# Kernel optimization log

Measured on AMD Instinct MI355X. Metric: run time of the kernel, lower is better.

The kernel has to match this reference:

```python
import jax, jax.numpy as jnp
import numpy as np

INPUT_DIM = 512
PROJ_DIM = 128
HIDDEN = INPUT_DIM // 2  # 256


def setup_inputs() -> dict:
    key = jax.random.key(0)
    ks = jax.random.split(key, 6)
    B = 8192
    s1 = 1.0 / np.sqrt(INPUT_DIM)
    s2 = 1.0 / np.sqrt(HIDDEN)
    return {
        "fused_text": jax.random.normal(ks[0], (B, INPUT_DIM), dtype=jnp.float32),
        "x": jax.random.normal(ks[1], (B, INPUT_DIM), dtype=jnp.float32),
        # generator layer 1: Linear(input_dim, input_dim//2), torch layout [out, in]
        "W1": jax.random.uniform(ks[2], (HIDDEN, INPUT_DIM), jnp.float32, -s1, s1),
        "b1": jax.random.uniform(ks[3], (HIDDEN,), jnp.float32, -s1, s1),
        # generator layer 2: Linear(input_dim//2, proj_dim * input_dim)
        "W2": jax.random.uniform(ks[4], (PROJ_DIM * INPUT_DIM, HIDDEN), jnp.float32, -s2, s2),
        "b2": jax.random.uniform(ks[5], (PROJ_DIM * INPUT_DIM,), jnp.float32, -s2, s2),
    }


def reference(fused_text, x, W1, b1, W2, b2):
    B = fused_text.shape[0]
    # hypernetwork generator MLP
    h = jax.nn.relu(fused_text @ W1.T + b1)          # [B, hidden]
    w_flat = h @ W2.T + b2                           # [B, proj_dim * input_dim]
    W = w_flat.reshape(B, PROJ_DIM, INPUT_DIM)       # per-sample weights
    # per-sample projection: bmm(W, x[..., None]).squeeze(-1)
    out = jnp.einsum("bpi,bi->bp", W, x)             # [B, proj_dim]
    return out
```

## Files before the change

kernel.cpp:

```cpp
#include <hip/hip_runtime.h>
#include <stdint.h>

#define B_SZ   8192
#define IN_DIM 512
#define HID    256
#define PROJ   128

typedef __attribute__((ext_vector_type(8))) short bf16x8;
typedef __attribute__((ext_vector_type(4))) float f32x4;

#define GLDS16(gp, lp) __builtin_amdgcn_global_load_lds( \
    (const __attribute__((address_space(1))) void*)(gp), \
    (__attribute__((address_space(3))) void*)(lp), 16, 0, 0)

__device__ __forceinline__ unsigned short f2bf(float f) {
    union { float f; uint32_t u; } c; c.f = f;
    uint32_t u = c.u;
    uint32_t r = (u + 0x7fffu + ((u >> 16) & 1u)) >> 16;
    return (unsigned short)r;
}
__device__ __forceinline__ float bfhi(uint32_t v) {
    union { uint32_t u; float f; } c; c.u = v & 0xffff0000u; return c.f;
}
__device__ __forceinline__ float bflo(uint32_t v) {
    union { uint32_t u; float f; } c; c.u = v << 16; return c.f;
}

__global__ __launch_bounds__(256) void k0_prep(
        const float4* __restrict__ W2, ushort4* __restrict__ W2b,
        const float* __restrict__ x, unsigned short* __restrict__ xTb) {
    __shared__ float tile[64][65];
    const int bid = blockIdx.x;
    if (bid < 2048) {
        const int nW2 = (PROJ * IN_DIM * HID) / 4;
        const int stride = 2048 * 256;
        for (int i = bid * 256 + threadIdx.x; i < nW2; i += stride) {
            float4 v = W2[i];
            ushort4 o;
            o.x = f2bf(v.x); o.y = f2bf(v.y); o.z = f2bf(v.z); o.w = f2bf(v.w);
            W2b[i] = o;
        }
    } else {
        const int tb = bid - 2048;
        const int bi = tb & 7, bb = tb >> 3;
        const int i0 = bi * 64, b0 = bb * 64;
        const int t = threadIdx.x;
        const int c = t & 63, r4 = t >> 6;
        #pragma unroll
        for (int rr = 0; rr < 64; rr += 4)
            tile[rr + r4][c] = x[(size_t)(b0 + rr + r4) * IN_DIM + i0 + c];
        __syncthreads();
        #pragma unroll
        for (int rr = 0; rr < 64; rr += 4)
            xTb[(size_t)(i0 + rr + r4) * B_SZ + b0 + c] = f2bf(tile[c][rr + r4]);
    }
}

__device__ __forceinline__ bf16x8 ld_cvt8(const float* __restrict__ s) {
    float4 a = *(const float4*)s;
    float4 b = *(const float4*)(s + 4);
    bf16x8 r;
    r[0] = (short)f2bf(a.x); r[1] = (short)f2bf(a.y);
    r[2] = (short)f2bf(a.z); r[3] = (short)f2bf(a.w);
    r[4] = (short)f2bf(b.x); r[5] = (short)f2bf(b.y);
    r[6] = (short)f2bf(b.z); r[7] = (short)f2bf(b.w);
    return r;
}

__global__ __launch_bounds__(256) void k1_hidden(
        const float* __restrict__ ft,
        const float* __restrict__ W1,
        const float* __restrict__ b1,
        unsigned short* __restrict__ hb) {
    const int lane = threadIdx.x & 63;
    const int wv   = threadIdx.x >> 6;
    const int l15  = lane & 15, q = lane >> 4;
    const int b0 = blockIdx.x * 32;
    const int n0 = wv * 64;

    f32x4 acc[2][4];
    const f32x4 z4 = {0.f, 0.f, 0.f, 0.f};
    #pragma unroll
    for (int mt = 0; mt < 2; ++mt)
        #pragma unroll
        for (int nt = 0; nt < 4; ++nt) acc[mt][nt] = z4;

    for (int kq = 0; kq < 16; ++kq) {
        const int koff = kq * 32 + q * 8;
        bf16x8 a[2], bb[4];
        #pragma unroll
        for (int mt = 0; mt < 2; ++mt)
            a[mt] = ld_cvt8(ft + (size_t)(b0 + mt*16 + l15) * IN_DIM + koff);
        #pragma unroll
        for (int nt = 0; nt < 4; ++nt)
            bb[nt] = ld_cvt8(W1 + (size_t)(n0 + nt*16 + l15) * IN_DIM + koff);
        #pragma unroll
        for (int mt = 0; mt < 2; ++mt)
            #pragma unroll
            for (int nt = 0; nt < 4; ++nt)
                acc[mt][nt] = __builtin_amdgcn_mfma_f32_16x16x32_bf16(
                    a[mt], bb[nt], acc[mt][nt], 0, 0, 0);
    }
    #pragma unroll
    for (int nt = 0; nt < 4; ++nt) {
        float bias = b1[n0 + nt*16 + l15];
        #pragma unroll
        for (int mt = 0; mt < 2; ++mt)
            #pragma unroll
            for (int r = 0; r < 4; ++r) {
                float v = acc[mt][nt][r] + bias;
                v = fmaxf(v, 0.f);
                hb[(size_t)(b0 + mt*16 + q*4 + r) * HID + n0 + nt*16 + l15] = f2bf(v);
            }
    }
}

__global__ __launch_bounds__(256) void k2_bias(
        const float* __restrict__ x,
        const float* __restrict__ b2,
        float* __restrict__ out) {
    const int lane = threadIdx.x & 63;
    const int wv   = threadIdx.x >> 6;
    const int l15  = lane & 15, q = lane >> 4;
    const int b0 = blockIdx.x * 32;
    const int n0 = wv * 32;

    f32x4 acc[2][2];
    const f32x4 z4 = {0.f, 0.f, 0.f, 0.f};
    #pragma unroll
    for (int mt = 0; mt < 2; ++mt)
        #pragma unroll
        for (int nt = 0; nt < 2; ++nt) acc[mt][nt] = z4;

    for (int kq = 0; kq < 16; ++kq) {
        const int koff = kq * 32 + q * 8;
        bf16x8 a[2], bb[2];
        #pragma unroll
        for (int mt = 0; mt < 2; ++mt)
            a[mt] = ld_cvt8(x + (size_t)(b0 + mt*16 + l15) * IN_DIM + koff);
        #pragma unroll
        for (int nt = 0; nt < 2; ++nt)
            bb[nt] = ld_cvt8(b2 + (size_t)(n0 + nt*16 + l15) * IN_DIM + koff);
        #pragma unroll
        for (int mt = 0; mt < 2; ++mt)
            #pragma unroll
            for (int nt = 0; nt < 2; ++nt)
                acc[mt][nt] = __builtin_amdgcn_mfma_f32_16x16x32_bf16(
                    a[mt], bb[nt], acc[mt][nt], 0, 0, 0);
    }
    #pragma unroll
    for (int mt = 0; mt < 2; ++mt)
        #pragma unroll
        for (int nt = 0; nt < 2; ++nt)
            #pragma unroll
            for (int r = 0; r < 4; ++r)
                out[(size_t)(b0 + mt*16 + q*4 + r) * PROJ + n0 + nt*16 + l15]
                    = acc[mt][nt][r];
}

__global__ __launch_bounds__(256, 3) void k3_main(
        const unsigned short* __restrict__ W2b,
        const unsigned short* __restrict__ hb,
        const unsigned short* __restrict__ xTb,
        float* __restrict__ out) {
    __shared__ unsigned short w2t[2][64 * 128];
    __shared__ unsigned short xt[2][32 * 128];
    const int tid  = threadIdx.x;
    const int lane = tid & 63;
    const int wv   = tid >> 6;
    const int l15  = lane & 15, q = lane >> 4;
    const int pgrp = blockIdx.x & 63;
    const int bsup = blockIdx.x >> 6;
    const int p0   = pgrp * 2;
    const int b0blk = bsup * 128;
    const int b0w  = b0blk + wv * 32;
    const f32x4 z4 = {0.f, 0.f, 0.f, 0.f};

    bf16x8 afr[2][8];
    #pragma unroll
    for (int mt = 0; mt < 2; ++mt) {
        const unsigned short* hrow = hb + (size_t)(b0w + mt*16 + l15) * HID + q * 8;
        #pragma unroll
        for (int kk = 0; kk < 8; ++kk)
            afr[mt][kk] = *(const bf16x8*)(hrow + kk * 32);
    }

    const int grow = lane >> 4;
    const int cbase = (lane & 15) ^ grow;
    const unsigned short* wsp[4];
    #pragma unroll
    for (int jj = 0; jj < 4; ++jj) {
        const int j   = wv*4 + jj;
        const int row = j*4 + grow;
        const int c   = cbase ^ (4*(jj & 1));
        wsp[jj] = W2b + ((size_t)(p0 + (row >> 5)) * IN_DIM + (row & 31)) * HID + c * 8;
    }
    const unsigned short* xsp[2];
    #pragma unroll
    for (int jj = 0; jj < 2; ++jj) {
        const int j2  = wv*2 + jj;
        const int row = j2*4 + (lane >> 4);
        const int g   = (lane & 15) ^ (row & 7);
        xsp[jj] = xTb + (size_t)row * B_SZ + b0blk + g * 8;
    }

    float oacc[2][2][4];
    #pragma unroll
    for (int pp = 0; pp < 2; ++pp)
        #pragma unroll
        for (int mt = 0; mt < 2; ++mt)
            #pragma unroll
            for (int r = 0; r < 4; ++r) oacc[pp][mt][r] = 0.f;

#define STAGE(BUFI, TT) do {                                              \
    const int _kh = (TT) >> 4, _ic = (TT) & 15;                           \
    const size_t _wadd = (size_t)(_ic * 32) * HID + _kh * 128;            \
    const size_t _xadd = (size_t)(_ic * 32) * B_SZ;                       \
    unsigned short* _Lw = &w2t[BUFI][0];                                  \
    unsigned short* _Lx = &xt[BUFI][0];                                   \
    _Pragma("unroll")                                                     \
    for (int _jj = 0; _jj < 4; ++_jj)                                     \
        GLDS16(wsp[_jj] + _wadd, _Lw + (wv*4 + _jj) * 512);               \
    _Pragma("unroll")                                                     \
    for (int _jj = 0; _jj < 2; ++_jj)                                     \
        GLDS16(xsp[_jj] + _xadd, _Lx + (wv*2 + _jj) * 512);               \
} while (0)

#define COMPUTE(KHC) do {                                                 \
    _Pragma("unroll")                                                     \
    for (int sub = 0; sub < 2; ++sub) {                                   \
        const int rloc = sub*16 + l15;                                    \
        uint2 xv[2];                                                      \
        _Pragma("unroll")                                                 \
        for (int mt = 0; mt < 2; ++mt) {                                  \
            const int gch = wv*4 + mt*2 + (q >> 1);                       \
            const int pos = gch ^ (rloc & 7);                             \
            xv[mt] = *(const uint2*)(Lx + rloc*128 + pos*8 + (q & 1)*4);  \
        }                                                                 \
        _Pragma("unroll")                                                 \
        for (int pp = 0; pp < 2; ++pp) {                                  \
            const unsigned short* Bp = Lw + (pp*32 + rloc) * 128;         \
            const int sw = rloc & 7;                                      \
            bf16x8 bfr[4];                                                \
            _Pragma("unroll")                                             \
            for (int kq = 0; kq < 4; ++kq)                                \
                bfr[kq] = *(const bf16x8*)(Bp + (((q + 4*kq) ^ sw)) * 8); \
            f32x4 D[2];                                                   \
            _Pragma("unroll")                                             \
            for (int mt = 0; mt < 2; ++mt)                                \
                D[mt] = __builtin_amdgcn_mfma_f32_16x16x32_bf16(          \
                    afr[mt][(KHC)*4 + 0], bfr[0], z4, 0, 0, 0);           \
            _Pragma("unroll")                                             \
            for (int kq = 1; kq < 4; ++kq)                                \
                _Pragma("unroll")                                         \
                for (int mt = 0; mt < 2; ++mt)                            \
                    D[mt] = __builtin_amdgcn_mfma_f32_16x16x32_bf16(      \
                        afr[mt][(KHC)*4 + kq], bfr[kq], D[mt], 0, 0, 0);  \
            _Pragma("unroll")                                             \
            for (int mt = 0; mt < 2; ++mt) {                              \
                oacc[pp][mt][0] = fmaf(D[mt][0], bflo(xv[mt].x), oacc[pp][mt][0]); \
                oacc[pp][mt][1] = fmaf(D[mt][1], bfhi(xv[mt].x), oacc[pp][mt][1]); \
                oacc[pp][mt][2] = fmaf(D[mt][2], bflo(xv[mt].y), oacc[pp][mt][2]); \
                oacc[pp][mt][3] = fmaf(D[mt][3], bfhi(xv[mt].y), oacc[pp][mt][3]); \
            }                                                             \
        }                                                                 \
    }                                                                     \
} while (0)

    STAGE(0, 0);
    STAGE(1, 1);

    #pragma unroll 1
    for (int t = 0; t < 32; ++t) {
        if (t < 31) asm volatile("s_waitcnt vmcnt(6)" ::: "memory");
        else        asm volatile("s_waitcnt vmcnt(0)" ::: "memory");
        __builtin_amdgcn_s_barrier();
        asm volatile("" ::: "memory");

        const unsigned short* Lw = &w2t[t & 1][0];
        const unsigned short* Lx = &xt[t & 1][0];
        if (t < 16) COMPUTE(0);
        else        COMPUTE(1);

        asm volatile("" ::: "memory");
        __builtin_amdgcn_s_barrier();
        asm volatile("" ::: "memory");

        if (t < 30) {
            const int tn = t + 2;
            STAGE(tn & 1, tn);
        }
    }
#undef STAGE
#undef COMPUTE

    #pragma unroll
    for (int pp = 0; pp < 2; ++pp)
        #pragma unroll
        for (int mt = 0; mt < 2; ++mt)
            #pragma unroll
            for (int r = 0; r < 4; ++r) {
                float v = oacc[pp][mt][r];
                v += __shfl_xor(v, 1, 16);
                v += __shfl_xor(v, 2, 16);
                v += __shfl_xor(v, 4, 16);
                v += __shfl_xor(v, 8, 16);
                if (l15 == 0)
                    out[(size_t)(b0w + mt*16 + q*4 + r) * PROJ + p0 + pp] += v;
            }
}

extern "C" void kernel_launch(void* const* d_in, const int* in_sizes, int n_in,
                              void* d_out, int out_size, void* d_ws, size_t ws_size,
                              hipStream_t stream) {
    const float* ft = (const float*)d_in[0];
    const float* x  = (const float*)d_in[1];
    const float* W1 = (const float*)d_in[2];
    const float* b1 = (const float*)d_in[3];
    const float* W2 = (const float*)d_in[4];
    const float* b2 = (const float*)d_in[5];
    float* out = (float*)d_out;

    char* ws = (char*)d_ws;
    unsigned short* W2b = (unsigned short*)(ws);
    unsigned short* hb  = (unsigned short*)(ws + 33554432);
    unsigned short* xTb = (unsigned short*)(ws + 37748736);

    hipLaunchKernelGGL(k0_prep, dim3(3072), dim3(256), 0, stream,
        (const float4*)W2, (ushort4*)W2b, x, xTb);
    hipLaunchKernelGGL(k1_hidden, dim3(256), dim3(256), 0, stream, ft, W1, b1, hb);
    hipLaunchKernelGGL(k2_bias, dim3(256), dim3(256), 0, stream, x, b2, out);
    hipLaunchKernelGGL(k3_main, dim3(4096), dim3(256), 0, stream, W2b, hb, xTb, out);
}
```

Before: 462.0 us.

## Retile main kernel to one projection row per block over 256 batch rows

Each block now computes one projection index for 256 batch rows, instead of two projection indices for 128 rows. Each W2 slice is therefore reused across twice as many samples, halving total W2 global traffic while doubling x traffic. The x tile is now single-buffered and loaded between barriers, so that load is not hidden behind compute, which is the main risk. The h fragments for the second K half are reloaded at the midpoint, and the LDS footprint is smaller, which cuts register and shared-memory pressure.

```diff
diff --git a/kernel.cpp b/kernel.cpp
--- a/kernel.cpp
+++ b/kernel.cpp
@@ -163,151 +163,151 @@
         const unsigned short* __restrict__ hb,
         const unsigned short* __restrict__ xTb,
         float* __restrict__ out) {
-    __shared__ unsigned short w2t[2][64 * 128];
-    __shared__ unsigned short xt[2][32 * 128];
+    __shared__ unsigned short w2t[2][2][32 * 64];
+    __shared__ unsigned short xt[32 * 256];
     const int tid  = threadIdx.x;
     const int lane = tid & 63;
     const int wv   = tid >> 6;
     const int l15  = lane & 15, q = lane >> 4;
-    const int pgrp = blockIdx.x & 63;
-    const int bsup = blockIdx.x >> 6;
-    const int p0   = pgrp * 2;
-    const int b0blk = bsup * 128;
-    const int b0w  = b0blk + wv * 32;
+    const int pgrp = blockIdx.x & 127;
+    const int bsup = blockIdx.x >> 7;
+    const int p0   = pgrp;
+    const int b0blk = bsup * 256;
+    const int b0w  = b0blk + wv * 64;
     const f32x4 z4 = {0.f, 0.f, 0.f, 0.f};
 
-    bf16x8 afr[2][8];
-    #pragma unroll
-    for (int mt = 0; mt < 2; ++mt) {
+    bf16x8 afr[4][4];
+    #pragma unroll
+    for (int mt = 0; mt < 4; ++mt) {
         const unsigned short* hrow = hb + (size_t)(b0w + mt*16 + l15) * HID + q * 8;
         #pragma unroll
-        for (int kk = 0; kk < 8; ++kk)
-            afr[mt][kk] = *(const bf16x8*)(hrow + kk * 32);
-    }
-
-    const int grow = lane >> 4;
-    const int cbase = (lane & 15) ^ grow;
-    const unsigned short* wsp[4];
+        for (int kq = 0; kq < 4; ++kq)
+            afr[mt][kq] = *(const bf16x8*)(hrow + kq * 32);
+    }
+
+    const unsigned short* wsp[2];
+    #pragma unroll
+    for (int jj = 0; jj < 2; ++jj) {
+        const int rl = wv*8 + (lane >> 3);
+        const int c  = (lane & 7) ^ (lane >> 3);
+        wsp[jj] = W2b + ((size_t)p0 * IN_DIM + rl) * HID + jj * 64 + c * 8;
+    }
+    const unsigned short* xsp[4];
     #pragma unroll
     for (int jj = 0; jj < 4; ++jj) {
-        const int j   = wv*4 + jj;
-        const int row = j*4 + grow;
-        const int c   = cbase ^ (4*(jj & 1));
-        wsp[jj] = W2b + ((size_t)(p0 + (row >> 5)) * IN_DIM + (row & 31)) * HID + c * 8;
-    }
-    const unsigned short* xsp[2];
-    #pragma unroll
-    for (int jj = 0; jj < 2; ++jj) {
-        const int j2  = wv*2 + jj;
-        const int row = j2*4 + (lane >> 4);
-        const int g   = (lane & 15) ^ (row & 7);
-        xsp[jj] = xTb + (size_t)row * B_SZ + b0blk + g * 8;
-    }
-
-    float oacc[2][2][4];
-    #pragma unroll
-    for (int pp = 0; pp < 2; ++pp)
-        #pragma unroll
-        for (int mt = 0; mt < 2; ++mt)
-            #pragma unroll
-            for (int r = 0; r < 4; ++r) oacc[pp][mt][r] = 0.f;
-
-#define STAGE(BUFI, TT) do {                                              \
+        const int r = wv*8 + jj*2 + (lane >> 5);
+        const int c = (lane & 31) ^ (r & 7);
+        xsp[jj] = xTb + (size_t)r * B_SZ + b0blk + c * 8;
+    }
+
+    float oacc[4][4];
+    #pragma unroll
+    for (int mt = 0; mt < 4; ++mt)
+        #pragma unroll
+        for (int r = 0; r < 4; ++r) oacc[mt][r] = 0.f;
+
+#define STAGE_W2(BUFI, TT) do {                                           \
     const int _kh = (TT) >> 4, _ic = (TT) & 15;                           \
-    const size_t _wadd = (size_t)(_ic * 32) * HID + _kh * 128;            \
-    const size_t _xadd = (size_t)(_ic * 32) * B_SZ;                       \
-    unsigned short* _Lw = &w2t[BUFI][0];                                  \
-    unsigned short* _Lx = &xt[BUFI][0];                                   \
+    const size_t _add = (size_t)(_ic * 32) * HID + _kh * 128;             \
+    _Pragma("unroll")                                                     \
+    for (int _jj = 0; _jj < 2; ++_jj)                                     \
+        GLDS16(wsp[_jj] + _add, &w2t[BUFI][_jj][wv * 512]);               \
+} while (0)
+
+#define STAGE_X(TT) do {                                                  \
+    const size_t _add = (size_t)(((TT) & 15) * 32) * B_SZ;                \
     _Pragma("unroll")                                                     \
     for (int _jj = 0; _jj < 4; ++_jj)                                     \
-        GLDS16(wsp[_jj] + _wadd, _Lw + (wv*4 + _jj) * 512);               \
-    _Pragma("unroll")                                                     \
-    for (int _jj = 0; _jj < 2; ++_jj)                                     \
-        GLDS16(xsp[_jj] + _xadd, _Lx + (wv*2 + _jj) * 512);               \
+        GLDS16(xsp[_jj] + _add, &xt[(wv*8 + _jj*2) * 256]);               \
 } while (0)
 
-#define COMPUTE(KHC) do {                                                 \
+#define COMPUTE() do {                                                    \
     _Pragma("unroll")                                                     \
     for (int sub = 0; sub < 2; ++sub) {                                   \
         const int rloc = sub*16 + l15;                                    \
-        uint2 xv[2];                                                      \
-        _Pragma("unroll")                                                 \
-        for (int mt = 0; mt < 2; ++mt) {                                  \
-            const int gch = wv*4 + mt*2 + (q >> 1);                       \
-            const int pos = gch ^ (rloc & 7);                             \
-            xv[mt] = *(const uint2*)(Lx + rloc*128 + pos*8 + (q & 1)*4);  \
+        const int sw   = rloc & 7;                                        \
+        uint2 xv[4];                                                      \
+        _Pragma("unroll")                                                 \
+        for (int mt = 0; mt < 4; ++mt) {                                  \
+            const int cc = wv*8 + mt*2 + (q >> 1);                        \
+            const int ss = cc ^ sw;                                       \
+            xv[mt] = *(const uint2*)(&xt[rloc*256 + ss*8 + (q & 1)*4]);   \
         }                                                                 \
-        _Pragma("unroll")                                                 \
-        for (int pp = 0; pp < 2; ++pp) {                                  \
-            const unsigned short* Bp = Lw + (pp*32 + rloc) * 128;         \
-            const int sw = rloc & 7;                                      \
-            bf16x8 bfr[4];                                                \
+        bf16x8 bfr[4];                                                    \
+        _Pragma("unroll")                                                 \
+        for (int kq = 0; kq < 4; ++kq) {                                  \
+            const int khf = kq >> 1;                                      \
+            const int ch  = (q + 4*(kq & 1)) ^ sw;                        \
+            bfr[kq] = *(const bf16x8*)(Lw + khf*2048 + rloc*64 + ch*8);   \
+        }                                                                 \
+        f32x4 D[4];                                                       \
+        _Pragma("unroll")                                                 \
+        for (int mt = 0; mt < 4; ++mt)                                    \
+            D[mt] = __builtin_amdgcn_mfma_f32_16x16x32_bf16(              \
+                afr[mt][0], bfr[0], z4, 0, 0, 0);                         \
+        _Pragma("unroll")                                                 \
+        for (int kq = 1; kq < 4; ++kq)                                    \
             _Pragma("unroll")                                             \
-            for (int kq = 0; kq < 4; ++kq)                                \
-                bfr[kq] = *(const bf16x8*)(Bp + (((q + 4*kq) ^ sw)) * 8); \
-            f32x4 D[2];                                                   \
-            _Pragma("unroll")                                             \
-            for (int mt = 0; mt < 2; ++mt)                                \
+            for (int mt = 0; mt < 4; ++mt)                                \
                 D[mt] = __builtin_amdgcn_mfma_f32_16x16x32_bf16(          \
-                    afr[mt][(KHC)*4 + 0], bfr[0], z4, 0, 0, 0);           \
-            _Pragma("unroll")                                             \
-            for (int kq = 1; kq < 4; ++kq)                                \
-                _Pragma("unroll")                                         \
-                for (int mt = 0; mt < 2; ++mt)                            \
-                    D[mt] = __builtin_amdgcn_mfma_f32_16x16x32_bf16(      \
-                        afr[mt][(KHC)*4 + kq], bfr[kq], D[mt], 0, 0, 0);  \
-            _Pragma("unroll")                                             \
-            for (int mt = 0; mt < 2; ++mt) {                              \
-                oacc[pp][mt][0] = fmaf(D[mt][0], bflo(xv[mt].x), oacc[pp][mt][0]); \
-                oacc[pp][mt][1] = fmaf(D[mt][1], bfhi(xv[mt].x), oacc[pp][mt][1]); \
-                oacc[pp][mt][2] = fmaf(D[mt][2], bflo(xv[mt].y), oacc[pp][mt][2]); \
-                oacc[pp][mt][3] = fmaf(D[mt][3], bfhi(xv[mt].y), oacc[pp][mt][3]); \
-            }                                                             \
+                    afr[mt][kq], bfr[kq], D[mt], 0, 0, 0);                \
+        _Pragma("unroll")                                                 \
+        for (int mt = 0; mt < 4; ++mt) {                                  \
+            oacc[mt][0] = fmaf(D[mt][0], bflo(xv[mt].x), oacc[mt][0]);    \
+            oacc[mt][1] = fmaf(D[mt][1], bfhi(xv[mt].x), oacc[mt][1]);    \
+            oacc[mt][2] = fmaf(D[mt][2], bflo(xv[mt].y), oacc[mt][2]);    \
+            oacc[mt][3] = fmaf(D[mt][3], bfhi(xv[mt].y), oacc[mt][3]);    \
         }                                                                 \
     }                                                                     \
 } while (0)
 
-    STAGE(0, 0);
-    STAGE(1, 1);
+    STAGE_W2(0, 0);
+    STAGE_X(0);
+    STAGE_W2(1, 1);
 
     #pragma unroll 1
     for (int t = 0; t < 32; ++t) {
-        if (t < 31) asm volatile("s_waitcnt vmcnt(6)" ::: "memory");
+        if (t < 31) asm volatile("s_waitcnt vmcnt(2)" ::: "memory");
         else        asm volatile("s_waitcnt vmcnt(0)" ::: "memory");
         __builtin_amdgcn_s_barrier();
         asm volatile("" ::: "memory");
 
-        const unsigned short* Lw = &w2t[t & 1][0];
-        const unsigned short* Lx = &xt[t & 1][0];
-        if (t < 16) COMPUTE(0);
-        else        COMPUTE(1);
+        const unsigned short* Lw = &w2t[t & 1][0][0];
+        COMPUTE();
 
         asm volatile("" ::: "memory");
         __builtin_amdgcn_s_barrier();
         asm volatile("" ::: "memory");
 
-        if (t < 30) {
-            const int tn = t + 2;
-            STAGE(tn & 1, tn);
+        if (t == 15) {
+            #pragma unroll
+            for (int mt = 0; mt < 4; ++mt) {
+                const unsigned short* hrow =
+                    hb + (size_t)(b0w + mt*16 + l15) * HID + 128 + q * 8;
+                #pragma unroll
+                for (int kq = 0; kq < 4; ++kq)
+                    afr[mt][kq] = *(const bf16x8*)(hrow + kq * 32);
+            }
         }
-    }
-#undef STAGE
+        if (t < 31) STAGE_X(t + 1);
+        if (t < 30) STAGE_W2(t & 1, t + 2);
+    }
+#undef STAGE_W2
+#undef STAGE_X
 #undef COMPUTE
 
     #pragma unroll
-    for (int pp = 0; pp < 2; ++pp)
-        #pragma unroll
-        for (int mt = 0; mt < 2; ++mt)
-            #pragma unroll
-            for (int r = 0; r < 4; ++r) {
-                float v = oacc[pp][mt][r];
-                v += __shfl_xor(v, 1, 16);
-                v += __shfl_xor(v, 2, 16);
-                v += __shfl_xor(v, 4, 16);
-                v += __shfl_xor(v, 8, 16);
-                if (l15 == 0)
-                    out[(size_t)(b0w + mt*16 + q*4 + r) * PROJ + p0 + pp] += v;
-            }
+    for (int mt = 0; mt < 4; ++mt)
+        #pragma unroll
+        for (int r = 0; r < 4; ++r) {
+            float v = oacc[mt][r];
+            v += __shfl_xor(v, 1, 16);
+            v += __shfl_xor(v, 2, 16);
+            v += __shfl_xor(v, 4, 16);
+            v += __shfl_xor(v, 8, 16);
+            if (l15 == 0)
+                out[(size_t)(b0w + mt*16 + q*4 + r) * PROJ + p0] += v;
+        }
 }
 
 extern "C" void kernel_launch(void* const* d_in, const int* in_sizes, int n_in,
```

After: 455.3 us. No clear change (-1.5%).
